# Performance work log

Measured on AMD Instinct MI355X. Metric: run time of the kernel, lower is better.

The kernel has to match this reference:

```python
import jax, jax.numpy as jnp
import numpy as np

B, L, DM, DH = 8, 2048, 1024, 1024


def setup_inputs() -> dict:
    key = jax.random.key(0)
    ks = jax.random.split(key, 10)
    s_dm = 1.0 / np.sqrt(DM)   # nn.Linear(d_model, *) init bound
    s_dh = 1.0 / np.sqrt(DH)   # nn.Linear(d_hidden, *) init bound
    u = lambda k, shp, s: jax.random.uniform(k, shp, jnp.float32, -s, s)
    return {
        "x": jax.random.normal(ks[0], (B, L, DM), jnp.float32),
        # A scaled by 0.01 so cumprod(exp(delta*A)) stays finite over L=2048
        "A": 0.01 * jax.random.normal(ks[1], (DH,), jnp.float32),
        "Bw": u(ks[2], (DH, DM), s_dm), "Bb": u(ks[3], (DH,), s_dm),
        "Cw": u(ks[4], (DM, DH), s_dh), "Cb": u(ks[5], (DM,), s_dh),
        "Dw": u(ks[6], (DM, DM), s_dm), "Db": u(ks[7], (DM,), s_dm),
        "dw": u(ks[8], (DH, DM), s_dm), "db": u(ks[9], (DH,), s_dm),
    }


def reference(x, A, Bw, Bb, Cw, Cb, Dw, Db, dw, db):
    # x: [B, L, DM]
    delta = jax.nn.softplus(jnp.einsum('bld,hd->blh', x, dw) + db)   # [B,L,DH]
    A_bar = jnp.exp(delta * A)                                        # [B,L,DH]
    B_bar = delta * (jnp.einsum('bld,hd->blh', x, Bw) + Bb)           # [B,L,DH]
    A_cum = jnp.cumprod(A_bar, axis=1)                                # [B,L,DH]
    h = jnp.cumsum(B_bar / A_cum, axis=1) * A_cum                     # [B,L,DH]
    out = jnp.einsum('blh,dh->bld', h, Cw) + Cb \
        + jnp.einsum('bld,ed->ble', x, Dw) + Db                       # [B,L,DM]
    return out
```

## Files before the change

kernel.cpp:

```cpp
#include <hip/hip_runtime.h>
#include <hip/hip_bf16.h>
#include <stdint.h>

#define DMODEL 1024
#define DHID   1024
#define NBATCH 8
#define LSEQ   2048
#define MROWS  (NBATCH * LSEQ)
#define KCAT   2048
#define CH     32
#define NCH    64
#define BH     (NBATCH * DHID)
#define CPT    4

typedef __attribute__((ext_vector_type(8))) short  short8;
typedef __attribute__((ext_vector_type(4))) short  s16x4;
typedef __attribute__((ext_vector_type(8))) __bf16 bf16x8;
typedef __attribute__((ext_vector_type(4))) float  f32x4;

__device__ __forceinline__ unsigned short f2bf(float f) {
  union { float f; unsigned int u; } v; v.f = f;
  unsigned int u = v.u;
  u += 0x7fffu + ((u >> 16) & 1u);
  return (unsigned short)(u >> 16);
}

__device__ __forceinline__ float bf2f(unsigned short s) {
  union { unsigned int u; float f; } v; v.u = ((unsigned int)s) << 16;
  return v.f;
}

__device__ __forceinline__ float softplus_f(float x) {
  return fmaxf(x, 0.f) + __logf(1.f + __expf(-fabsf(x)));
}

__device__ __forceinline__ short8 pack8(float4 a, float4 b) {
  short8 o;
  o[0] = (short)f2bf(a.x); o[1] = (short)f2bf(a.y);
  o[2] = (short)f2bf(a.z); o[3] = (short)f2bf(a.w);
  o[4] = (short)f2bf(b.x); o[5] = (short)f2bf(b.y);
  o[6] = (short)f2bf(b.z); o[7] = (short)f2bf(b.w);
  return o;
}

__global__ __launch_bounds__(256)
void cast_all_kernel(const float* __restrict__ x,
                     const float* __restrict__ dw, const float* __restrict__ Bw,
                     const float* __restrict__ Cw, const float* __restrict__ Dw,
                     unsigned short* __restrict__ A2,
                     unsigned short* __restrict__ W1, unsigned short* __restrict__ W2) {
  const size_t MX = (size_t)MROWS * 1024;
  const size_t M1 = (size_t)1024 * 1024;
  size_t i8 = ((size_t)blockIdx.x * 256 + threadIdx.x) * 8;
  if (i8 < MX) {
    size_t row = i8 >> 10; int col = (int)(i8 & 1023);
    const float4* p = (const float4*)(x + i8);
    *(short8*)(A2 + row * (size_t)KCAT + 1024 + col) = pack8(p[0], p[1]);
  } else if (i8 < MX + 2 * M1) {
    size_t k = i8 - MX;
    size_t h = k >> 11;
    int c = (int)(k & 1023);
    const float* src = ((k >> 10) & 1) ? (Bw + h * 1024 + c) : (dw + h * 1024 + c);
    const float4* p = (const float4*)src;
    *(short8*)(W1 + k) = pack8(p[0], p[1]);
  } else {
    size_t k = i8 - MX - 2 * M1;
    size_t d = k >> 11; int c = (int)(k & 2047);
    const float* src = (c < 1024) ? (Cw + d * 1024 + c) : (Dw + d * 1024 + (c - 1024));
    const float4* p = (const float4*)src;
    *(short8*)(W2 + k) = pack8(p[0], p[1]);
  }
}

__device__ __forceinline__ void stage_tile(const unsigned short* g0, int ld,
                                           unsigned short* s0, int t, int lane) {
#pragma unroll
  for (int half = 0; half < 2; ++half) {
    int c = t + half * 256;
    const unsigned short* g = g0 + (size_t)(c >> 2) * ld + (c & 3) * 8;
    unsigned short* s = s0 + ((size_t)(t - lane) + half * 256) * 8;
    __builtin_amdgcn_global_load_lds(
        (const __attribute__((address_space(1))) unsigned int*)g,
        (__attribute__((address_space(3))) unsigned int*)s, 16, 0, 0);
  }
}

__global__ __launch_bounds__(256, 4)
void gemm_bt(const unsigned short* __restrict__ A, int lda,
             const unsigned short* __restrict__ B, int ldb,
             void* __restrict__ Cp, int ldc, int K, int mode,
             const float* __restrict__ bias0, const float* __restrict__ bias1) {
  __shared__ __align__(16) unsigned short As[128 * 32];
  __shared__ __align__(16) unsigned short Bs[128 * 32];
  const int t = threadIdx.x;
  const int lane = t & 63, wave = t >> 6;
  const int quad = lane >> 4, l16 = lane & 15;

  const int Nt = gridDim.x, Mt = gridDim.y;
  int bid = blockIdx.y * Nt + blockIdx.x;
  int xcd = bid & 7;
  int slot = bid >> 3;
  int lm = slot / Nt;
  int ln = slot - lm * Nt;
  const int m0 = (xcd * (Mt >> 3) + lm) * 128;
  const int n0 = ln * 128;

  const int wm = (wave & 1) * 64, wn = (wave >> 1) * 64;

  const unsigned short* Ab = A + (size_t)m0 * lda;
  const unsigned short* Bb = B + (size_t)n0 * ldb;

  f32x4 acc[4][4] = {};

  for (int k0 = 0; k0 < K; k0 += 32) {
    stage_tile(Ab + k0, lda, As, t, lane);
    stage_tile(Bb + k0, ldb, Bs, t, lane);
    __syncthreads();
    short8 af[4], bfr[4];
#pragma unroll
    for (int i = 0; i < 4; ++i)
      af[i] = *(const short8*)(As + ((size_t)(wm + i * 16 + l16)) * 32 + quad * 8);
#pragma unroll
    for (int j = 0; j < 4; ++j)
      bfr[j] = *(const short8*)(Bs + ((size_t)(wn + j * 16 + l16)) * 32 + quad * 8);
#pragma unroll
    for (int i = 0; i < 4; ++i)
#pragma unroll
      for (int j = 0; j < 4; ++j)
        acc[i][j] = __builtin_amdgcn_mfma_f32_16x16x32_bf16(
            __builtin_bit_cast(bf16x8, af[i]),
            __builtin_bit_cast(bf16x8, bfr[j]), acc[i][j], 0, 0, 0);
    __syncthreads();
  }

  if (mode == 0) {
    float* C = (float*)Cp;
#pragma unroll
    for (int i = 0; i < 4; ++i)
#pragma unroll
      for (int j = 0; j < 4; ++j) {
        int n = n0 + wn + j * 16 + l16;
        int mb = m0 + wm + i * 16 + quad * 4;
        float badd = bias0[n] + bias1[n];
#pragma unroll
        for (int r = 0; r < 4; ++r)
          C[(size_t)(mb + r) * ldc + n] = acc[i][j][r] + badd;
      }
  } else {
    unsigned short* C16 = (unsigned short*)Cp;
#pragma unroll
    for (int i = 0; i < 4; ++i)
#pragma unroll
      for (int j = 0; j < 4; ++j) {
        int n = n0 + wn + j * 16 + l16;
        int mb = m0 + wm + i * 16 + quad * 4;
        int h = n >> 1;
        bool isd = (n & 1) == 0;
        float bias = isd ? bias0[h] : bias1[h];
#pragma unroll
        for (int r = 0; r < 4; ++r) {
          float v = acc[i][j][r] + bias;
          float d = softplus_f(v);
          float dn = __shfl_xor(d, 1);
          float ov = isd ? d : dn * v;
          C16[(size_t)(mb + r) * ldc + n] = f2bf(ov);
        }
      }
  }
}

__global__ __launch_bounds__(256)
void scan_carry_kernel(const unsigned short* __restrict__ G1,
                       const float* __restrict__ Av, float2* __restrict__ carr) {
  int t = blockIdx.x * 256 + threadIdx.x;
  int ho = t & 255, chunk = (t >> 8) & (NCH - 1), b = t >> 14;
  int h0 = ho << 2;
  float4 A0 = *(const float4*)(Av + h0);
  float Ah[4] = {A0.x, A0.y, A0.z, A0.w};
  const unsigned short* base = G1 + ((size_t)(b * LSEQ + chunk * CH)) * KCAT + 2 * h0;
  float hs[4] = {}, sd[4] = {};
  short8 v0 = *(const short8*)(base);
  short8 v1 = *(const short8*)(base + KCAT);
#pragma unroll 4
  for (int l = 0; l < CH; ++l) {
    short8 v2 = v1;
    if (l + 2 < CH)
      v2 = *(const short8*)(base + (size_t)(l + 2) * KCAT);
#pragma unroll
    for (int j = 0; j < 4; ++j) {
      float d  = bf2f((unsigned short)v0[2 * j]);
      float bb = bf2f((unsigned short)v0[2 * j + 1]);
      sd[j] += d;
      hs[j] = fmaf(__expf(d * Ah[j]), hs[j], bb);
    }
    v0 = v1; v1 = v2;
  }
  float2* cb = carr + (size_t)chunk * BH + b * 1024 + h0;
#pragma unroll
  for (int j = 0; j < 4; ++j)
    cb[j] = make_float2(__expf(Ah[j] * sd[j]), hs[j]);
}

__global__ __launch_bounds__(256)
void scan_comb_kernel(const float2* __restrict__ carr, float* __restrict__ Hc) {
  int t = blockIdx.x * 256 + threadIdx.x;
  float2 buf[8];
#pragma unroll
  for (int i = 0; i < 8; ++i) buf[i] = carr[(size_t)i * BH + t];
  float H = 0.f;
#pragma unroll
  for (int c = 0; c < NCH; ++c) {
    float2 ah = buf[c & 7];
    if (c + 8 < NCH) buf[c & 7] = carr[(size_t)(c + 8) * BH + t];
    Hc[(size_t)c * BH + t] = H;
    H = fmaf(ah.x, H, ah.y);
  }
}

__global__ __launch_bounds__(256)
void scan_final_kernel(const unsigned short* __restrict__ G1,
                       const float* __restrict__ Av, const float* __restrict__ Hc,
                       unsigned short* __restrict__ A2) {
  int t = blockIdx.x * 256 + threadIdx.x;
  int ho = t & 255, chunk = (t >> 8) & (NCH - 1), b = t >> 14;
  int h0 = ho << 2;
  float4 A0 = *(const float4*)(Av + h0);
  float Ah[4] = {A0.x, A0.y, A0.z, A0.w};
  const unsigned short* base = G1 + ((size_t)(b * LSEQ + chunk * CH)) * KCAT + 2 * h0;
  unsigned short* obase = A2 + ((size_t)(b * LSEQ + chunk * CH)) * KCAT + h0;
  const float* hb = Hc + (size_t)chunk * BH + b * 1024 + h0;
  float hs[4];
#pragma unroll
  for (int j = 0; j < 4; ++j) hs[j] = hb[j];
  short8 v0 = *(const short8*)(base);
  short8 v1 = *(const short8*)(base + KCAT);
#pragma unroll 4
  for (int l = 0; l < CH; ++l) {
    short8 v2 = v1;
    if (l + 2 < CH)
      v2 = *(const short8*)(base + (size_t)(l + 2) * KCAT);
    s16x4 o;
#pragma unroll
    for (int j = 0; j < 4; ++j) {
      float d  = bf2f((unsigned short)v0[2 * j]);
      float bb = bf2f((unsigned short)v0[2 * j + 1]);
      hs[j] = fmaf(__expf(d * Ah[j]), hs[j], bb);
      o[j] = (short)f2bf(hs[j]);
    }
    *(s16x4*)(obase + (size_t)l * KCAT) = o;
    v0 = v1; v1 = v2;
  }
}

extern "C" void kernel_launch(void* const* d_in, const int* in_sizes, int n_in,
                              void* d_out, int out_size, void* d_ws, size_t ws_size,
                              hipStream_t stream) {
  const float* x  = (const float*)d_in[0];
  const float* Av = (const float*)d_in[1];
  const float* Bw = (const float*)d_in[2];
  const float* Bb = (const float*)d_in[3];
  const float* Cw = (const float*)d_in[4];
  const float* Cb = (const float*)d_in[5];
  const float* Dw = (const float*)d_in[6];
  const float* Db = (const float*)d_in[7];
  const float* dw = (const float*)d_in[8];
  const float* db = (const float*)d_in[9];
  float* out = (float*)d_out;

  const size_t sz_big = (size_t)MROWS * KCAT * 2;
  const size_t sz_w   = (size_t)2048 * 1024 * 2;
  const size_t sz_hc  = (size_t)NCH * BH * 4;
  const size_t need = 2 * sz_big + 2 * sz_w + sz_hc;
  if (ws_size < need) return;

  char* w = (char*)d_ws;
  unsigned short* A2 = (unsigned short*)w; w += sz_big;
  unsigned short* G1 = (unsigned short*)w; w += sz_big;
  unsigned short* W1 = (unsigned short*)w; w += sz_w;
  unsigned short* W2 = (unsigned short*)w; w += sz_w;
  float* Hc = (float*)w;                   w += sz_hc;
  float2* carr = (float2*)W1;

  const size_t cast_elems = (size_t)MROWS * 1024 + 2 * (size_t)2048 * 1024;
  cast_all_kernel<<<(int)(cast_elems / (256 * 8)), 256, 0, stream>>>(
      x, dw, Bw, Cw, Dw, A2, W1, W2);

  dim3 g1(KCAT / 128, MROWS / 128);
  gemm_bt<<<g1, 256, 0, stream>>>(A2 + 1024, KCAT, W1, 1024, G1, KCAT, 1024, 2,
                                  db, Bb);

  scan_carry_kernel<<<(NBATCH * NCH * (DHID / CPT)) / 256, 256, 0, stream>>>(
      G1, Av, carr);
  scan_comb_kernel<<<BH / 256, 256, 0, stream>>>(carr, Hc);
  scan_final_kernel<<<(NBATCH * NCH * (DHID / CPT)) / 256, 256, 0, stream>>>(
      G1, Av, Hc, A2);

  dim3 g2(DMODEL / 128, MROWS / 128);
  gemm_bt<<<g2, 256, 0, stream>>>(A2, KCAT, W2, KCAT, out, DMODEL, KCAT, 0, Cb, Db);
}
```

Before: 341.3 us.

## Fuse chunk-carry combine into final scan kernel, dropping separate combine launch

Removes the scan_comb kernel that serially combined per-chunk carries into an Hc buffer. Each thread of the final scan now recomputes its own starting state by folding the carries of all preceding chunks, prefetching the next carry pair. This saves one launch and the Hc write/read round trip. In exchange it adds redundant work that grows with chunk index, up to 63 serial FMAs and float4 loads per thread, which creates load imbalance across blocks.

```diff
diff --git a/kernel.cpp b/kernel.cpp
--- a/kernel.cpp
+++ b/kernel.cpp
@@ -202,24 +202,8 @@
 }
 
 __global__ __launch_bounds__(256)
-void scan_comb_kernel(const float2* __restrict__ carr, float* __restrict__ Hc) {
-  int t = blockIdx.x * 256 + threadIdx.x;
-  float2 buf[8];
-#pragma unroll
-  for (int i = 0; i < 8; ++i) buf[i] = carr[(size_t)i * BH + t];
-  float H = 0.f;
-#pragma unroll
-  for (int c = 0; c < NCH; ++c) {
-    float2 ah = buf[c & 7];
-    if (c + 8 < NCH) buf[c & 7] = carr[(size_t)(c + 8) * BH + t];
-    Hc[(size_t)c * BH + t] = H;
-    H = fmaf(ah.x, H, ah.y);
-  }
-}
-
-__global__ __launch_bounds__(256)
 void scan_final_kernel(const unsigned short* __restrict__ G1,
-                       const float* __restrict__ Av, const float* __restrict__ Hc,
+                       const float* __restrict__ Av, const float2* __restrict__ carr,
                        unsigned short* __restrict__ A2) {
   int t = blockIdx.x * 256 + threadIdx.x;
   int ho = t & 255, chunk = (t >> 8) & (NCH - 1), b = t >> 14;
@@ -228,12 +212,31 @@
   float Ah[4] = {A0.x, A0.y, A0.z, A0.w};
   const unsigned short* base = G1 + ((size_t)(b * LSEQ + chunk * CH)) * KCAT + 2 * h0;
   unsigned short* obase = A2 + ((size_t)(b * LSEQ + chunk * CH)) * KCAT + h0;
-  const float* hb = Hc + (size_t)chunk * BH + b * 1024 + h0;
-  float hs[4];
-#pragma unroll
-  for (int j = 0; j < 4; ++j) hs[j] = hb[j];
+
   short8 v0 = *(const short8*)(base);
   short8 v1 = *(const short8*)(base + KCAT);
+
+  float hs[4] = {0.f, 0.f, 0.f, 0.f};
+  const float2* cb = carr + b * 1024 + h0;
+  float4 pA = {}, pB = {};
+  if (chunk > 0) {
+    pA = *(const float4*)(cb);
+    pB = *(const float4*)(cb + 2);
+  }
+  for (int c = 0; c < chunk; ++c) {
+    float4 nA = {}, nB = {};
+    if (c + 1 < chunk) {
+      const float2* nc = cb + (size_t)(c + 1) * BH;
+      nA = *(const float4*)(nc);
+      nB = *(const float4*)(nc + 2);
+    }
+    hs[0] = fmaf(pA.x, hs[0], pA.y);
+    hs[1] = fmaf(pA.z, hs[1], pA.w);
+    hs[2] = fmaf(pB.x, hs[2], pB.y);
+    hs[3] = fmaf(pB.z, hs[3], pB.w);
+    pA = nA; pB = nB;
+  }
+
 #pragma unroll 4
   for (int l = 0; l < CH; ++l) {
     short8 v2 = v1;
@@ -278,7 +281,6 @@
   unsigned short* G1 = (unsigned short*)w; w += sz_big;
   unsigned short* W1 = (unsigned short*)w; w += sz_w;
   unsigned short* W2 = (unsigned short*)w; w += sz_w;
-  float* Hc = (float*)w;                   w += sz_hc;
   float2* carr = (float2*)W1;
 
   const size_t cast_elems = (size_t)MROWS * 1024 + 2 * (size_t)2048 * 1024;
@@ -291,9 +293,8 @@
 
   scan_carry_kernel<<<(NBATCH * NCH * (DHID / CPT)) / 256, 256, 0, stream>>>(
       G1, Av, carr);
-  scan_comb_kernel<<<BH / 256, 256, 0, stream>>>(carr, Hc);
   scan_final_kernel<<<(NBATCH * NCH * (DHID / CPT)) / 256, 256, 0, stream>>>(
-      G1, Av, Hc, A2);
+      G1, Av, carr, A2);
 
   dim3 g2(DMODEL / 128, MROWS / 128);
   gemm_bt<<<g2, 256, 0, stream>>>(A2, KCAT, W2, KCAT, out, DMODEL, KCAT, 0, Cb, Db);
```

New measurement: 351.8 us. 3.1% more time.
